# Kernel tuning notes

Hardware: AMD Instinct MI355X
Metric: run time of the kernel (lower is better)

Reference implementation:

```python
import jax, jax.numpy as jnp
import numpy as np

C = 256
NUM_HEADS = 8
FFN_HIDDEN = C * 2  # ffn_expand=2
EPS = 1e-5


def setup_inputs() -> dict:
    key = jax.random.key(0)
    ks = jax.random.split(key, 12)
    B, H, W = 16, 64, 64
    s = 0.02
    return {
        "optical": jax.random.normal(ks[0], (B, C, H, W), jnp.float32),
        "sar": jax.random.normal(ks[1], (B, C, H, W), jnp.float32),
        "g_opt": jnp.ones((C,), jnp.float32),
        "b_opt": jnp.zeros((C,), jnp.float32),
        "g_sar": jnp.ones((C,), jnp.float32),
        "b_sar": jnp.zeros((C,), jnp.float32),
        "Wq": jax.random.normal(ks[2], (C, C), jnp.float32) * s,
        "Wk": jax.random.normal(ks[3], (C, C), jnp.float32) * s,
        "Wv": jax.random.normal(ks[4], (C, C), jnp.float32) * s,
        "Wo": jax.random.normal(ks[5], (C, C), jnp.float32) * s,
        "g_ffn": jnp.ones((C,), jnp.float32),
        "b_ffn": jnp.zeros((C,), jnp.float32),
        "W1": jax.random.normal(ks[6], (2 * FFN_HIDDEN, C), jnp.float32) * s,
        "b1": jnp.zeros((2 * FFN_HIDDEN,), jnp.float32),
        "W2": jax.random.normal(ks[7], (C, FFN_HIDDEN), jnp.float32) * s,
        "b2": jnp.zeros((C,), jnp.float32),
    }


def _ln(x, g, b):
    # LayerNorm over channel axis of (B, C, H, W), biased variance, eps=1e-5
    mu = jnp.mean(x, axis=1, keepdims=True)
    var = jnp.mean(jnp.square(x - mu), axis=1, keepdims=True)
    xn = (x - mu) * jax.lax.rsqrt(var + EPS)
    return xn * g[None, :, None, None] + b[None, :, None, None]


def _proj(x, Wmat):
    # 1x1 conv == channel matmul
    return jnp.einsum('oc,bchw->bohw', Wmat, x)


def reference(optical, sar, g_opt, b_opt, g_sar, b_sar, Wq, Wk, Wv, Wo,
              g_ffn, b_ffn, W1, b1, W2, b2):
    B, Cc, H, W = optical.shape
    hc = Cc // NUM_HEADS
    L = H * W
    scale = hc ** -0.5

    opt_n = _ln(optical, g_opt, b_opt)
    sar_n = _ln(sar, g_sar, b_sar)

    # channel (transposed) attention: contraction over spatial L
    q = _proj(opt_n, Wq).reshape(B, NUM_HEADS, hc, L)
    k = _proj(sar_n, Wk).reshape(B, NUM_HEADS, hc, L)
    v = _proj(sar_n, Wv).reshape(B, NUM_HEADS, hc, L)
    A = jax.nn.softmax(jnp.einsum('bhcl,bhdl->bhcd', q, k) * scale, axis=-1)
    attn = jnp.einsum('bhcd,bhdl->bhcl', A, v).reshape(B, Cc, H, W)
    x = optical + _proj(attn, Wo)

    # SimpleGate FFN
    h = _ln(x, g_ffn, b_ffn)
    h = _proj(h, W1) + b1[None, :, None, None]
    h1, h2 = jnp.split(h, 2, axis=1)
    h = _proj(h1 * h2, W2) + b2[None, :, None, None]
    return x + h
```

## Files before the change

kernel.cpp:

```cpp
#include <hip/hip_runtime.h>
#include <hip/hip_bf16.h>

typedef __bf16 bf16;
typedef __attribute__((ext_vector_type(8))) __bf16 bf16x8;
typedef __attribute__((ext_vector_type(4))) __bf16 bf16x4;
typedef __attribute__((ext_vector_type(4))) float f32x4;
typedef __attribute__((ext_vector_type(16))) float f32x16;

#define LSP 4096
#define CCH 256

__device__ __forceinline__ void gl2lds16(const bf16* g, bf16* l) {
  __builtin_amdgcn_global_load_lds(
      (const __attribute__((address_space(1))) unsigned int*)g,
      (__attribute__((address_space(3))) unsigned int*)l, 16, 0, 0);
}

__device__ __forceinline__ f32x4 mfma16(bf16x8 a, bf16x8 b, f32x4 c) {
  return __builtin_amdgcn_mfma_f32_16x16x32_bf16(a, b, c, 0, 0, 0);
}
__device__ __forceinline__ f32x16 mfma32(bf16x8 a, bf16x8 b, f32x16 c) {
  return __builtin_amdgcn_mfma_f32_32x32x16_bf16(a, b, c, 0, 0, 0);
}

__global__ __launch_bounds__(256) void cvt_w_kernel(
    const float* __restrict__ wq, const float* __restrict__ wk,
    const float* __restrict__ wv, const float* __restrict__ wo,
    const float* __restrict__ w1, const float* __restrict__ w2,
    bf16* __restrict__ out) {
  int e = blockIdx.x * 256 + threadIdx.x;
  if (e < 65536)        { out[e] = (bf16)wq[e]; }
  else if (e < 131072)  { out[e] = (bf16)wk[e - 65536]; }
  else if (e < 196608)  {
    int e2 = e - 131072;
    int och = e2 >> 8, cin = e2 & 255;
    out[131072 + cin * 256 + och] = (bf16)wv[e2];
  }
  else if (e < 262144)  { out[e] = (bf16)wo[e - 196608]; }
  else if (e < 524288)  {
    int e2 = e - 262144;
    int m = e2 >> 8, k = e2 & 255;
    int mp = (m < 512) ? (2 * m) : (2 * (m - 512) + 1);
    out[262144 + mp * 256 + k] = (bf16)w1[e2];
  }
  else                  { out[e] = (bf16)w2[e - 524288]; }
}

__global__ __launch_bounds__(256) void ln_cl_kernel(
    const float* __restrict__ x, const float* __restrict__ gam,
    const float* __restrict__ bet, bf16* __restrict__ out_cl) {
  int p = blockIdx.x * 256 + threadIdx.x;
  int b = p >> 12, l = p & 4095;
  const float* px = x + (size_t)b * CCH * LSP + l;
  float s = 0.f, s2 = 0.f;
  #pragma unroll 16
  for (int c = 0; c < CCH; ++c) {
    float v = px[(size_t)c * LSP];
    s += v; s2 += v * v;
  }
  float mean = s * (1.f / 256.f);
  float var  = s2 * (1.f / 256.f) - mean * mean;
  float rs   = rsqrtf(var + 1e-5f);
  bf16* po = out_cl + (size_t)b * CCH * LSP + l;
  #pragma unroll 16
  for (int c = 0; c < CCH; ++c) {
    float v = px[(size_t)c * LSP];
    po[(size_t)c * LSP] = (bf16)((v - mean) * rs * gam[c] + bet[c]);
  }
}

__global__ __launch_bounds__(256) void ln_dual_kernel(
    const float* __restrict__ x, const float* __restrict__ gam,
    const float* __restrict__ bet, bf16* __restrict__ out_cl,
    bf16* __restrict__ out_lc) {
  int p = blockIdx.x * 256 + threadIdx.x;
  int b = p >> 12, l = p & 4095;
  const float* px = x + (size_t)b * CCH * LSP + l;
  float s = 0.f, s2 = 0.f;
  #pragma unroll 16
  for (int c = 0; c < CCH; ++c) {
    float v = px[(size_t)c * LSP];
    s += v; s2 += v * v;
  }
  float mean = s * (1.f / 256.f);
  float var  = s2 * (1.f / 256.f) - mean * mean;
  float rs   = rsqrtf(var + 1e-5f);
  bf16* pcl = out_cl + (size_t)b * CCH * LSP + l;
  bf16* plc = out_lc + (size_t)p * CCH;
  #pragma unroll 8
  for (int c0 = 0; c0 < CCH; c0 += 4) {
    bf16x4 o;
    #pragma unroll
    for (int i = 0; i < 4; ++i) {
      float v = px[(size_t)(c0 + i) * LSP];
      bf16 r = (bf16)((v - mean) * rs * gam[c0 + i] + bet[c0 + i]);
      o[i] = r;
      pcl[(size_t)(c0 + i) * LSP] = r;
    }
    *(bf16x4*)&plc[c0] = o;
  }
}

__global__ __launch_bounds__(256) void gram_kernel(
    const bf16* __restrict__ sar_cl, const bf16* __restrict__ opt_cl,
    float* __restrict__ part) {
  const int tile = blockIdx.x, chunk = blockIdx.y, b = blockIdx.z;
  const int tid = threadIdx.x, lane = tid & 63, w = tid >> 6;
  const int j0 = (tile >> 1) * 128 + (w >> 1) * 64;
  const int i0 = (tile & 1) * 128 + (w & 1) * 64;
  const int l0 = chunk * 1024;
  const bf16* sj = sar_cl + ((size_t)b * CCH + j0 + (lane & 31)) * LSP + l0;
  const bf16* oi = opt_cl + ((size_t)b * CCH + i0 + (lane & 31)) * LSP + l0;
  f32x16 acc[2][2];
  #pragma unroll
  for (int mt = 0; mt < 2; ++mt)
    #pragma unroll
    for (int nt = 0; nt < 2; ++nt)
      #pragma unroll
      for (int r = 0; r < 16; ++r) acc[mt][nt][r] = 0.f;
  #pragma unroll 4
  for (int ks = 0; ks < 64; ++ks) {
    int lofs = ks * 16 + (lane >> 5) * 8;
    bf16x8 a0 = *(const bf16x8*)&sj[lofs];
    bf16x8 a1 = *(const bf16x8*)&sj[32 * LSP + lofs];
    bf16x8 b0 = *(const bf16x8*)&oi[lofs];
    bf16x8 b1 = *(const bf16x8*)&oi[32 * LSP + lofs];
    acc[0][0] = mfma32(a0, b0, acc[0][0]);
    acc[0][1] = mfma32(a0, b1, acc[0][1]);
    acc[1][0] = mfma32(a1, b0, acc[1][0]);
    acc[1][1] = mfma32(a1, b1, acc[1][1]);
  }
  float* op = part + ((size_t)chunk * 16 + b) * 65536;
  #pragma unroll
  for (int mt = 0; mt < 2; ++mt)
    #pragma unroll
    for (int nt = 0; nt < 2; ++nt)
      #pragma unroll
      for (int r = 0; r < 16; ++r) {
        int row = j0 + mt * 32 + (r & 3) + 8 * (r >> 2) + 4 * (lane >> 5);
        int col = i0 + nt * 32 + (lane & 31);
        op[(size_t)row * 256 + col] = acc[mt][nt][r];
      }
}

__global__ __launch_bounds__(256) void greduce_kernel(
    const float* __restrict__ part, bf16* __restrict__ G2) {
  size_t e = ((size_t)blockIdx.x * 256 + threadIdx.x) * 8;
  float a[8];
  #pragma unroll
  for (int i = 0; i < 8; ++i) a[i] = 0.f;
  #pragma unroll
  for (int ch = 0; ch < 4; ++ch) {
    f32x4 p0 = *(const f32x4*)&part[ch * 1048576ull + e];
    f32x4 p1 = *(const f32x4*)&part[ch * 1048576ull + e + 4];
    #pragma unroll
    for (int i = 0; i < 4; ++i) { a[i] += p0[i]; a[4 + i] += p1[i]; }
  }
  bf16x8 o;
  #pragma unroll
  for (int i = 0; i < 8; ++i) o[i] = (bf16)a[i];
  *(bf16x8*)&G2[e] = o;
}

__global__ __launch_bounds__(256) void fold2_kernel(
    const bf16* __restrict__ G2, const bf16* __restrict__ Wq,
    const bf16* __restrict__ Wk, const bf16* __restrict__ WvT,
    bf16* __restrict__ UT) {
  const int bh = blockIdx.x;
  const int b = bh >> 3, h = bh & 7;
  const int tid = threadIdx.x, lane = tid & 63, w = tid >> 6;
  __shared__ bf16 M1[32 * 256];
  __shared__ float Sp[4][1024];
  __shared__ float S[1024];
  __shared__ bf16 P[1024];

  const bf16* gq = Wq + (size_t)(h * 32) * 256;
  const bf16* g2b = G2 + (size_t)b * 65536;
  #pragma unroll
  for (int mt = 0; mt < 2; ++mt)
    #pragma unroll
    for (int nt = 0; nt < 4; ++nt) {
      f32x4 acc = {0.f, 0.f, 0.f, 0.f};
      #pragma unroll
      for (int ks = 0; ks < 8; ++ks) {
        bf16x8 a = *(const bf16x8*)&gq[(size_t)(mt * 16 + (lane & 15)) * 256 +
                                       ks * 32 + (lane >> 4) * 8];
        bf16x8 bb = *(const bf16x8*)&g2b[
            (size_t)(w * 64 + nt * 16 + (lane & 15)) * 256 + ks * 32 +
            (lane >> 4) * 8];
        acc = mfma16(a, bb, acc);
      }
      #pragma unroll
      for (int r = 0; r < 4; ++r)
        M1[(mt * 16 + (lane >> 4) * 4 + r) * 256 + w * 64 + nt * 16 +
           (lane & 15)] = (bf16)acc[r];
    }
  __syncthreads();

  const bf16* gk = Wk + (size_t)(h * 32) * 256;
  #pragma unroll
  for (int mt = 0; mt < 2; ++mt)
    #pragma unroll
    for (int dt = 0; dt < 2; ++dt) {
      f32x4 acc = {0.f, 0.f, 0.f, 0.f};
      #pragma unroll
      for (int kk = 0; kk < 2; ++kk) {
        bf16x8 a = *(const bf16x8*)&M1[(mt * 16 + (lane & 15)) * 256 + w * 64 +
                                       kk * 32 + (lane >> 4) * 8];
        bf16x8 bb = *(const bf16x8*)&gk[(size_t)(dt * 16 + (lane & 15)) * 256 +
                                        w * 64 + kk * 32 + (lane >> 4) * 8];
        acc = mfma16(a, bb, acc);
      }
      #pragma unroll
      for (int r = 0; r < 4; ++r)
        Sp[w][(mt * 16 + (lane >> 4) * 4 + r) * 32 + dt * 16 + (lane & 15)] =
            acc[r];
    }
  __syncthreads();
  #pragma unroll
  for (int i = 0; i < 4; ++i) {
    int e = tid + 256 * i;
    S[e] = (Sp[0][e] + Sp[1][e] + Sp[2][e] + Sp[3][e]) * 0.17677669529663687f;
  }
  __syncthreads();
  if (tid < 32) {
    float m = -1e30f;
    #pragma unroll
    for (int d = 0; d < 32; ++d) m = fmaxf(m, S[tid * 32 + d]);
    float sum = 0.f;
    float ex[32];
    #pragma unroll
    for (int d = 0; d < 32; ++d) {
      ex[d] = __expf(S[tid * 32 + d] - m);
      sum += ex[d];
    }
    float inv = 1.f / sum;
    #pragma unroll
    for (int d = 0; d < 32; ++d) P[tid * 32 + d] = (bf16)(ex[d] * inv);
  }
  __syncthreads();

  bf16x8 bfrag[2];
  #pragma unroll
  for (int ct = 0; ct < 2; ++ct)
    bfrag[ct] =
        *(const bf16x8*)&P[(ct * 16 + (lane & 15)) * 32 + (lane >> 4) * 8];
  bf16* outb = UT + (size_t)b * 65536 + h * 32;
  #pragma unroll
  for (int t = 0; t < 4; ++t) {
    int cin16 = w * 64 + t * 16;
    bf16x8 afrag = *(const bf16x8*)&WvT[(size_t)(cin16 + (lane & 15)) * 256 +
                                        h * 32 + (lane >> 4) * 8];
    #pragma unroll
    for (int ct = 0; ct < 2; ++ct) {
      f32x4 acc = {0.f, 0.f, 0.f, 0.f};
      acc = mfma16(afrag, bfrag[ct], acc);
      int c = ct * 16 + (lane & 15);
      int cinr = cin16 + (lane >> 4) * 4;
      #pragma unroll
      for (int r = 0; r < 4; ++r)
        outb[(size_t)(cinr + r) * 256 + c] = (bf16)acc[r];
    }
  }
}

__global__ __launch_bounds__(256) void wfold_kernel(
    const bf16* __restrict__ Aw, const bf16* __restrict__ Bx,
    bf16* __restrict__ outp) {
  const int tid = threadIdx.x;
  const int lane = tid & 63;
  const int wave = tid >> 6;
  const int wr = wave >> 1, wc = wave & 1;
  const int l0 = blockIdx.x * 128;
  const int m0 = blockIdx.y * 128;
  const int b  = blockIdx.z;
  constexpr int NB = 4096;
  __shared__ bf16 smem[4 * NB];
  bf16* As = smem;
  bf16* Bs = smem + 2 * NB;
  const bf16* Ag = Aw + (size_t)m0 * 256;
  const bf16* Bg = Bx + ((size_t)b * 256 + l0) * 256;
  auto stage = [&](int buf, int k0) {
    #pragma unroll
    for (int i = 0; i < 2; ++i) {
      int ch = i * 256 + tid;
      int r  = ch >> 2;
      int c8 = (ch & 3) * 8;
      gl2lds16(Ag + (size_t)r * 256 + k0 + c8, As + buf * NB + ch * 8);
      gl2lds16(Bg + (size_t)r * 256 + k0 + c8, Bs + buf * NB + ch * 8);
    }
  };
  f32x4 acc[4][4];
  #pragma unroll
  for (int mi = 0; mi < 4; ++mi)
    #pragma unroll
    for (int ni = 0; ni < 4; ++ni)
      #pragma unroll
      for (int r = 0; r < 4; ++r) acc[mi][ni][r] = 0.f;
  stage(0, 0);
  for (int kt = 0; kt < 8; ++kt) {
    __syncthreads();
    if (kt + 1 < 8) stage((kt + 1) & 1, (kt + 1) * 32);
    const bf16* Ab = As + (kt & 1) * NB;
    const bf16* Bb = Bs + (kt & 1) * NB;
    bf16x8 af[4], bfr[4];
    #pragma unroll
    for (int mi = 0; mi < 4; ++mi)
      af[mi] = *(const bf16x8*)&Ab[(wr * 64 + mi * 16 + (lane & 15)) * 32 +
                                   (lane >> 4) * 8];
    #pragma unroll
    for (int ni = 0; ni < 4; ++ni)
      bfr[ni] = *(const bf16x8*)&Bb[(wc * 64 + ni * 16 + (lane & 15)) * 32 +
                                    (lane >> 4) * 8];
    #pragma unroll
    for (int mi = 0; mi < 4; ++mi)
      #pragma unroll
      for (int ni = 0; ni < 4; ++ni)
        acc[mi][ni] = mfma16(af[mi], bfr[ni], acc[mi][ni]);
  }
  const int mq = m0 + wr * 64 + (lane >> 4) * 4;
  const int lq = l0 + wc * 64 + (lane & 15);
  #pragma unroll
  for (int mi = 0; mi < 4; ++mi)
    #pragma unroll
    for (int ni = 0; ni < 4; ++ni) {
      int l = lq + ni * 16, mb = mq + mi * 16;
      #pragma unroll
      for (int r = 0; r < 4; ++r)
        outp[((size_t)b * 256 + mb + r) * 256 + l] = (bf16)acc[mi][ni][r];
    }
}

__global__ __launch_bounds__(256) void xgemm_ln_kernel(
    const bf16* __restrict__ Wfold, const bf16* __restrict__ sar_lc,
    const float* __restrict__ optical, const float* __restrict__ gff,
    const float* __restrict__ bff, float* __restrict__ xbuf,
    bf16* __restrict__ hn) {
  const int tid = threadIdx.x, lane = tid & 63, w = tid >> 6;
  const int l0 = blockIdx.x * 64;
  const int b  = blockIdx.y;
  __shared__ bf16 As[2][256 * 32];
  __shared__ bf16 Bs[2][64 * 32];
  __shared__ float red[2][4][64];

  const bf16* Ag = Wfold + (size_t)b * 65536;
  const bf16* Bg = sar_lc + ((size_t)b * LSP + l0) * CCH;

  auto stage = [&](int buf, int k0) {
    #pragma unroll
    for (int i = 0; i < 4; ++i) {
      int ch = i * 256 + tid;
      int r = ch >> 2, c8 = (ch & 3) * 8;
      gl2lds16(Ag + (size_t)r * 256 + k0 + c8, &As[buf][ch * 8]);
    }
    {
      int r = tid >> 2, c8 = (tid & 3) * 8;
      gl2lds16(Bg + (size_t)r * 256 + k0 + c8, &Bs[buf][tid * 8]);
    }
  };

  f32x4 acc[4][4];
  #pragma unroll
  for (int mi = 0; mi < 4; ++mi)
    #pragma unroll
    for (int ni = 0; ni < 4; ++ni)
      #pragma unroll
      for (int r = 0; r < 4; ++r) acc[mi][ni][r] = 0.f;

  stage(0, 0);
  for (int kt = 0; kt < 8; ++kt) {
    __syncthreads();
    if (kt < 7) stage((kt + 1) & 1, (kt + 1) * 32);
    const bf16* Ab = As[kt & 1];
    const bf16* Bb = Bs[kt & 1];
    bf16x8 af[4], bfr[4];
    #pragma unroll
    for (int mi = 0; mi < 4; ++mi)
      af[mi] = *(const bf16x8*)&Ab[(w * 64 + mi * 16 + (lane & 15)) * 32 +
                                   (lane >> 4) * 8];
    #pragma unroll
    for (int ni = 0; ni < 4; ++ni)
      bfr[ni] = *(const bf16x8*)&Bb[(ni * 16 + (lane & 15)) * 32 +
                                    (lane >> 4) * 8];
    #pragma unroll
    for (int mi = 0; mi < 4; ++mi)
      #pragma unroll
      for (int ni = 0; ni < 4; ++ni)
        acc[mi][ni] = mfma16(af[mi], bfr[ni], acc[mi][ni]);
  }

  const int cb = w * 64 + (lane >> 4) * 4;
  const int lb = l0 + (lane & 15);
  float s[4], q[4];
  #pragma unroll
  for (int ni = 0; ni < 4; ++ni) { s[ni] = 0.f; q[ni] = 0.f; }
  #pragma unroll
  for (int mi = 0; mi < 4; ++mi)
    #pragma unroll
    for (int ni = 0; ni < 4; ++ni) {
      int c = cb + mi * 16, l = lb + ni * 16;
      #pragma unroll
      for (int r = 0; r < 4; ++r) {
        float v = acc[mi][ni][r] + optical[((size_t)b * CCH + c + r) * LSP + l];
        acc[mi][ni][r] = v;
        s[ni] += v; q[ni] += v * v;
      }
    }
  #pragma unroll
  for (int ni = 0; ni < 4; ++ni) {
    s[ni] += __shfl_xor(s[ni], 16);
    s[ni] += __shfl_xor(s[ni], 32);
    q[ni] += __shfl_xor(q[ni], 16);
    q[ni] += __shfl_xor(q[ni], 32);
  }
  if ((lane >> 4) == 0) {
    #pragma unroll
    for (int ni = 0; ni < 4; ++ni) {
      red[0][w][ni * 16 + (lane & 15)] = s[ni];
      red[1][w][ni * 16 + (lane & 15)] = q[ni];
    }
  }
  __syncthreads();
  float mu[4], rsg[4];
  #pragma unroll
  for (int ni = 0; ni < 4; ++ni) {
    int ll = ni * 16 + (lane & 15);
    float S4 = red[0][0][ll] + red[0][1][ll] + red[0][2][ll] + red[0][3][ll];
    float Q4 = red[1][0][ll] + red[1][1][ll] + red[1][2][ll] + red[1][3][ll];
    float m = S4 * (1.f / 256.f);
    mu[ni] = m;
    rsg[ni] = rsqrtf(Q4 * (1.f / 256.f) - m * m + 1e-5f);
  }
  #pragma unroll
  for (int mi = 0; mi < 4; ++mi) {
    int c = cb + mi * 16;
    f32x4 g4 = *(const f32x4*)&gff[c];
    f32x4 b4 = *(const f32x4*)&bff[c];
    #pragma unroll
    for (int ni = 0; ni < 4; ++ni) {
      int l = lb + ni * 16;
      f32x4 xv = acc[mi][ni];
      *(f32x4*)&xbuf[((size_t)b * LSP + l) * CCH + c] = xv;
      bf16x4 o;
      #pragma unroll
      for (int r = 0; r < 4; ++r)
        o[r] = (bf16)((xv[r] - mu[ni]) * rsg[ni] * g4[r] + b4[r]);
      *(bf16x4*)&hn[((size_t)b * LSP + l) * CCH + c] = o;
    }
  }
}

template <int KEL, int MODE>
__global__ __launch_bounds__(512, 2) void ffn_gemm_kernel(
    const bf16* __restrict__ Aw, const bf16* __restrict__ Bx,
    void* __restrict__ outp, const float* __restrict__ res,
    const float* __restrict__ bias) {
  constexpr int LDSB = (MODE == 1) ? 135168 : 131072;
  __shared__ __align__(16) char smem_raw[LDSB];
  const int tid = threadIdx.x;
  const int lane = tid & 63;
  const int wave = tid >> 6;
  const int wr = wave >> 2;
  const int wc = wave & 3;
  const int l0 = blockIdx.x * 256;
  const int m0 = blockIdx.y * 256;
  const int b  = blockIdx.z;

  char* ldsA0 = smem_raw;
  char* ldsB0 = smem_raw + 32768;
  char* ldsA1 = smem_raw + 65536;
  char* ldsB1 = smem_raw + 98304;

  const bf16* Ag = Aw + (size_t)m0 * KEL;
  const bf16* Bg = Bx + ((size_t)b * LSP + l0) * KEL;

  auto STAGE = [&](const bf16* gsrc, char* ldst, int par, int kt) {
    #pragma unroll
    for (int i = 0; i < 2; ++i) {
      int qi = i * 512 + tid;
      int r  = ((qi >> 7) << 5) + (par << 4) + ((qi >> 3) & 15);
      int cl = (qi & 7) ^ ((qi >> 3) & 7);
      int p  = ((qi >> 7) << 8) + (par << 7) + (qi & 127);
      gl2lds16(gsrc + (size_t)r * KEL + kt * 64 + cl * 8,
               (bf16*)(ldst + p * 16));
    }
  };

  f32x4 acc[8][4];
  #pragma unroll
  for (int mi = 0; mi < 8; ++mi)
    #pragma unroll
    for (int ni = 0; ni < 4; ++ni)
      #pragma unroll
      for (int r = 0; r < 4; ++r) acc[mi][ni][r] = 0.f;

  bf16x8 af[4][2], bf[2][2];
  const int col0 = (((lane >> 4) << 4)) ^ ((lane & 7) << 4);
  const int col1 = col0 ^ 64;
  const int arow_off = (lane & 15) * 128;

#define LOAD_FRAGS(BUFA, BUFB, MP, NP)                                        \
  {                                                                           \
    const char* Ab_ = (BUFA);                                                 \
    const char* Bb_ = (BUFB);                                                 \
    _Pragma("unroll") for (int j = 0; j < 4; ++j) {                           \
      int rb = (wr * 128 + ((MP) + 2 * j) * 16) * 128 + arow_off;             \
      af[j][0] = *(const bf16x8*)(Ab_ + rb + col0);                           \
      af[j][1] = *(const bf16x8*)(Ab_ + rb + col1);                           \
    }                                                                         \
    _Pragma("unroll") for (int i = 0; i < 2; ++i) {                           \
      int rb = (wc * 64 + ((NP) + 2 * i) * 16) * 128 + arow_off;              \
      bf[i][0] = *(const bf16x8*)(Bb_ + rb + col0);                           \
      bf[i][1] = *(const bf16x8*)(Bb_ + rb + col1);                           \
    }                                                                         \
  }

#define DO_MFMA(MP, NP)                                                       \
  _Pragma("unroll") for (int j = 0; j < 4; ++j)                               \
  _Pragma("unroll") for (int i = 0; i < 2; ++i) {                             \
    acc[(MP) + 2 * j][(NP) + 2 * i] =                                         \
        mfma16(af[j][0], bf[i][0], acc[(MP) + 2 * j][(NP) + 2 * i]);          \
    acc[(MP) + 2 * j][(NP) + 2 * i] =                                         \
        mfma16(af[j][1], bf[i][1], acc[(MP) + 2 * j][(NP) + 2 * i]);          \
  }

#define PHASE(BUFA, BUFB, MP, NP, STG)                                        \
  asm volatile("s_waitcnt vmcnt(6)" ::: "memory");                            \
  __builtin_amdgcn_s_barrier();                                               \
  __builtin_amdgcn_sched_barrier(0);                                          \
  LOAD_FRAGS(BUFA, BUFB, MP, NP);                                             \
  STG;                                                                        \
  asm volatile("s_waitcnt lgkmcnt(0)" ::: "memory");                          \
  __builtin_amdgcn_sched_barrier(0);                                          \
  __builtin_amdgcn_s_setprio(1);                                              \
  DO_MFMA(MP, NP);                                                            \
  __builtin_amdgcn_s_setprio(0);

  STAGE(Ag, ldsA0, 0, 0);
  STAGE(Ag, ldsA0, 1, 0);
  STAGE(Bg, ldsB0, 0, 0);
  STAGE(Bg, ldsB0, 1, 0);
  STAGE(Ag, ldsA1, 0, 1);
  STAGE(Bg, ldsB1, 0, 1);

  constexpr int NITER = KEL / 128;
  for (int t = 0; t < NITER; ++t) {
    const int kt1 = 2 * t + 1;
    PHASE(ldsA0, ldsB0, 0, 0, STAGE(Ag, ldsA1, 1, kt1));
    PHASE(ldsA0, ldsB0, 0, 1, STAGE(Bg, ldsB1, 1, kt1));
    PHASE(ldsA0, ldsB0, 1, 0, STAGE(Ag, ldsA0, 0, kt1 + 1));
    PHASE(ldsA0, ldsB0, 1, 1, STAGE(Bg, ldsB0, 0, kt1 + 1));
    PHASE(ldsA1, ldsB1, 0, 0, STAGE(Ag, ldsA0, 1, kt1 + 1));
    PHASE(ldsA1, ldsB1, 0, 1, STAGE(Bg, ldsB0, 1, kt1 + 1));
    PHASE(ldsA1, ldsB1, 1, 0, STAGE(Ag, ldsA1, 0, kt1 + 2));
    PHASE(ldsA1, ldsB1, 1, 1, STAGE(Bg, ldsB1, 0, kt1 + 2));
  }
#undef PHASE
#undef DO_MFMA
#undef LOAD_FRAGS

  asm volatile("s_waitcnt vmcnt(0)" ::: "memory");
  __syncthreads();

  if constexpr (MODE == 0) {
    bf16* g_lds = (bf16*)smem_raw;
    const int lq = wc * 64 + (lane & 15);
    const int qq = (lane >> 4);
    #pragma unroll
    for (int mi = 0; mi < 8; ++mi) {
      int a0 = wr * 64 + mi * 8 + qq * 2;
      int ag = (m0 >> 1) + a0;
      float b10 = bias[ag], b1h0 = bias[ag + 512];
      float b11 = bias[ag + 1], b1h1 = bias[ag + 1 + 512];
      #pragma unroll
      for (int ni = 0; ni < 4; ++ni) {
        int l = lq + ni * 16;
        float g0 = (acc[mi][ni][0] + b10) * (acc[mi][ni][1] + b1h0);
        float g1 = (acc[mi][ni][2] + b11) * (acc[mi][ni][3] + b1h1);
        bf16 gv0 = (bf16)g0, gv1 = (bf16)g1;
        unsigned u = ((unsigned)*(unsigned short*)&gv1 << 16) |
                     (unsigned)*(unsigned short*)&gv0;
        *(unsigned*)&g_lds[l * 136 + a0] = u;
      }
    }
    __syncthreads();
    bf16* out = (bf16*)outp;
    const int gy = blockIdx.y * 128;
    #pragma unroll
    for (int it = 0; it < 8; ++it) {
      int cid = it * 512 + tid;
      int l = cid >> 4, ch = cid & 15;
      bf16x8 v = *(const bf16x8*)&g_lds[l * 136 + ch * 8];
      *(bf16x8*)&out[((size_t)b * LSP + l0 + l) * 512 + gy + ch * 8] = v;
    }
  } else {
    float* lds_f = (float*)smem_raw;
    float* out = (float*)outp;
    const int lq = wc * 64 + (lane & 15);
    const int qq = (lane >> 4);
    #pragma unroll
    for (int round = 0; round < 2; ++round) {
      if (wr == round) {
        #pragma unroll
        for (int mi = 0; mi < 8; ++mi) {
          int c0 = mi * 16 + qq * 4;
          f32x4 b4 = *(const f32x4*)&bias[round * 128 + c0];
          #pragma unroll
          for (int ni = 0; ni < 4; ++ni) {
            int l = lq + ni * 16;
            f32x4 xr = *(const f32x4*)&res[((size_t)b * LSP + l0 + l) * CCH +
                                           round * 128 + c0];
            #pragma unroll
            for (int r = 0; r < 4; ++r)
              lds_f[(c0 + r) * 260 + l] = acc[mi][ni][r] + b4[r] + xr[r];
          }
        }
      }
      __syncthreads();
      #pragma unroll
      for (int it = 0; it < 16; ++it) {
        int cid = it * 512 + tid;
        int c = cid >> 6, lch = cid & 63;
        f32x4 v = *(const f32x4*)&lds_f[c * 260 + lch * 4];
        *(f32x4*)&out[((size_t)b * CCH + round * 128 + c) * LSP + l0 +
                      lch * 4] = v;
      }
      __syncthreads();
    }
  }
}

extern "C" void kernel_launch(void* const* d_in, const int* in_sizes, int n_in,
                              void* d_out, int out_size, void* d_ws,
                              size_t ws_size, hipStream_t stream) {
  const float* optical = (const float*)d_in[0];
  const float* sar     = (const float*)d_in[1];
  const float* g_opt   = (const float*)d_in[2];
  const float* b_opt   = (const float*)d_in[3];
  const float* g_sar   = (const float*)d_in[4];
  const float* b_sar   = (const float*)d_in[5];
  const float* Wq      = (const float*)d_in[6];
  const float* Wk      = (const float*)d_in[7];
  const float* Wv      = (const float*)d_in[8];
  const float* Wo      = (const float*)d_in[9];
  const float* g_ffn   = (const float*)d_in[10];
  const float* b_ffn   = (const float*)d_in[11];
  const float* W1      = (const float*)d_in[12];
  const float* b1      = (const float*)d_in[13];
  const float* W2      = (const float*)d_in[14];
  const float* b2      = (const float*)d_in[15];

  char* ws = (char*)d_ws;
  bf16* wbf  = (bf16*)ws;
  bf16* Wqb  = wbf;
  bf16* Wkb  = wbf + 65536;
  bf16* WvTb = wbf + 131072;
  bf16* Wob  = wbf + 196608;
  bf16* W1b  = wbf + 262144;
  bf16* W2b  = wbf + 524288;

  size_t off = 2ull * 1024 * 1024;
  const size_t T16 = 16ull * LSP * CCH * 2;
  bf16* opt_ncl = (bf16*)(ws + off); off += T16;
  bf16* sar_ncl = (bf16*)(ws + off); off += T16;
  bf16* sar_nlc = (bf16*)(ws + off); off += T16;
  bf16* hn      = (bf16*)(ws + off); off += T16;
  float* xbuf   = (float*)(ws + off); off += 2 * T16;
  float* Gpart  = (float*)(ws + off); off += 16ull * 1024 * 1024;
  bf16* G2b     = (bf16*)(ws + off); off += 4ull * 1024 * 1024;
  bf16* UTb     = (bf16*)(ws + off); off += 2ull * 1024 * 1024;
  bf16* Wfoldb  = (bf16*)(ws + off); off += 2ull * 1024 * 1024;
  bf16* gbuf = opt_ncl;

  dim3 blk(256);
  cvt_w_kernel<<<2560, blk, 0, stream>>>(Wq, Wk, Wv, Wo, W1, W2, wbf);
  ln_cl_kernel<<<256, blk, 0, stream>>>(optical, g_opt, b_opt, opt_ncl);
  ln_dual_kernel<<<256, blk, 0, stream>>>(sar, g_sar, b_sar, sar_ncl, sar_nlc);
  gram_kernel<<<dim3(4, 4, 16), blk, 0, stream>>>(sar_ncl, opt_ncl, Gpart);
  greduce_kernel<<<512, blk, 0, stream>>>(Gpart, G2b);
  fold2_kernel<<<128, blk, 0, stream>>>(G2b, Wqb, Wkb, WvTb, UTb);
  wfold_kernel<<<dim3(2, 2, 16), blk, 0, stream>>>(Wob, UTb, Wfoldb);
  xgemm_ln_kernel<<<dim3(64, 16), blk, 0, stream>>>(Wfoldb, sar_nlc, optical,
                                                    g_ffn, b_ffn, xbuf, hn);
  ffn_gemm_kernel<256, 0><<<dim3(16, 4, 16), dim3(512), 0, stream>>>(
      W1b, hn, gbuf, nullptr, b1);
  ffn_gemm_kernel<512, 1><<<dim3(16, 1, 16), dim3(512), 0, stream>>>(
      W2b, gbuf, (float*)d_out, xbuf, b2);
}
```

Measured before the change: 310.2 us.

## Replace per-pixel LayerNorm kernels with LDS-tiled, vectorized, swizzled LN kernel

Result: faster. 281.7 us (-9.2%).

```diff
diff --git a/kernel.cpp b/kernel.cpp
--- a/kernel.cpp
+++ b/kernel.cpp
@@ -46,58 +46,91 @@
   else                  { out[e] = (bf16)w2[e - 524288]; }
 }
 
-__global__ __launch_bounds__(256) void ln_cl_kernel(
-    const float* __restrict__ x, const float* __restrict__ gam,
-    const float* __restrict__ bet, bf16* __restrict__ out_cl) {
-  int p = blockIdx.x * 256 + threadIdx.x;
-  int b = p >> 12, l = p & 4095;
-  const float* px = x + (size_t)b * CCH * LSP + l;
-  float s = 0.f, s2 = 0.f;
-  #pragma unroll 16
-  for (int c = 0; c < CCH; ++c) {
-    float v = px[(size_t)c * LSP];
-    s += v; s2 += v * v;
-  }
-  float mean = s * (1.f / 256.f);
-  float var  = s2 * (1.f / 256.f) - mean * mean;
-  float rs   = rsqrtf(var + 1e-5f);
-  bf16* po = out_cl + (size_t)b * CCH * LSP + l;
-  #pragma unroll 16
-  for (int c = 0; c < CCH; ++c) {
-    float v = px[(size_t)c * LSP];
-    po[(size_t)c * LSP] = (bf16)((v - mean) * rs * gam[c] + bet[c]);
-  }
-}
-
-__global__ __launch_bounds__(256) void ln_dual_kernel(
+template <int DUAL>
+__global__ __launch_bounds__(256) void ln_tile_kernel(
     const float* __restrict__ x, const float* __restrict__ gam,
     const float* __restrict__ bet, bf16* __restrict__ out_cl,
     bf16* __restrict__ out_lc) {
-  int p = blockIdx.x * 256 + threadIdx.x;
-  int b = p >> 12, l = p & 4095;
-  const float* px = x + (size_t)b * CCH * LSP + l;
-  float s = 0.f, s2 = 0.f;
-  #pragma unroll 16
-  for (int c = 0; c < CCH; ++c) {
-    float v = px[(size_t)c * LSP];
-    s += v; s2 += v * v;
-  }
-  float mean = s * (1.f / 256.f);
-  float var  = s2 * (1.f / 256.f) - mean * mean;
-  float rs   = rsqrtf(var + 1e-5f);
-  bf16* pcl = out_cl + (size_t)b * CCH * LSP + l;
-  bf16* plc = out_lc + (size_t)p * CCH;
-  #pragma unroll 8
-  for (int c0 = 0; c0 < CCH; c0 += 4) {
-    bf16x4 o;
-    #pragma unroll
-    for (int i = 0; i < 4; ++i) {
-      float v = px[(size_t)(c0 + i) * LSP];
-      bf16 r = (bf16)((v - mean) * rs * gam[c0 + i] + bet[c0 + i]);
-      o[i] = r;
-      pcl[(size_t)(c0 + i) * LSP] = r;
-    }
-    *(bf16x4*)&plc[c0] = o;
+  const int l0 = blockIdx.x * 64;
+  const int b  = blockIdx.y;
+  const int tid = threadIdx.x;
+  __shared__ bf16 Tt[256 * 64];
+  __shared__ float red[2][16][64];
+  __shared__ float mu_s[64], rs_s[64];
+
+  const float* px = x + (size_t)b * CCH * LSP + l0;
+  const int colq = (tid & 15) * 4;
+  f32x4 s = {0.f, 0.f, 0.f, 0.f}, q = {0.f, 0.f, 0.f, 0.f};
+  #pragma unroll
+  for (int it = 0; it < 16; ++it) {
+    int c = it * 16 + (tid >> 4);
+    f32x4 v = *(const f32x4*)&px[(size_t)c * LSP + colq];
+    s += v;
+    q += v * v;
+    bf16x4 h;
+    #pragma unroll
+    for (int j = 0; j < 4; ++j) h[j] = (bf16)v[j];
+    int colp = colq ^ (((c >> 3) & 7) << 3);
+    *(bf16x4*)&Tt[c * 64 + colp] = h;
+  }
+  #pragma unroll
+  for (int j = 0; j < 4; ++j) {
+    red[0][tid >> 4][colq + j] = s[j];
+    red[1][tid >> 4][colq + j] = q[j];
+  }
+  __syncthreads();
+  if (tid < 64) {
+    float S = 0.f, Q = 0.f;
+    #pragma unroll
+    for (int k = 0; k < 16; ++k) { S += red[0][k][tid]; Q += red[1][k][tid]; }
+    float m = S * (1.f / 256.f);
+    mu_s[tid] = m;
+    rs_s[tid] = rsqrtf(Q * (1.f / 256.f) - m * m + 1e-5f);
+  }
+  __syncthreads();
+
+  #pragma unroll
+  for (int it = 0; it < 8; ++it) {
+    int ch = it * 256 + tid;
+    int c = ch >> 3, col8 = (ch & 7) * 8;
+    int colp = col8 ^ (((c >> 3) & 7) << 3);
+    bf16x8 h = *(const bf16x8*)&Tt[c * 64 + colp];
+    f32x4 m0 = *(const f32x4*)&mu_s[col8];
+    f32x4 m1 = *(const f32x4*)&mu_s[col8 + 4];
+    f32x4 r0 = *(const f32x4*)&rs_s[col8];
+    f32x4 r1 = *(const f32x4*)&rs_s[col8 + 4];
+    float g = gam[c], be = bet[c];
+    bf16x8 o;
+    #pragma unroll
+    for (int j = 0; j < 4; ++j) {
+      o[j]     = (bf16)(((float)h[j] - m0[j]) * r0[j] * g + be);
+      o[4 + j] = (bf16)(((float)h[4 + j] - m1[j]) * r1[j] * g + be);
+    }
+    *(bf16x8*)&out_cl[((size_t)b * CCH + c) * LSP + l0 + col8] = o;
+  }
+
+  if constexpr (DUAL) {
+    #pragma unroll
+    for (int it = 0; it < 8; ++it) {
+      int ch = it * 256 + tid;
+      int l = ch >> 5, cch = ch & 31;
+      int c0 = cch * 8;
+      int lp = l ^ ((cch & 7) << 3);
+      float mu = mu_s[l], rs = rs_s[l];
+      f32x4 g0 = *(const f32x4*)&gam[c0];
+      f32x4 g1 = *(const f32x4*)&gam[c0 + 4];
+      f32x4 b0 = *(const f32x4*)&bet[c0];
+      f32x4 b1 = *(const f32x4*)&bet[c0 + 4];
+      bf16x8 o;
+      #pragma unroll
+      for (int j = 0; j < 4; ++j) {
+        float h0 = (float)Tt[(c0 + j) * 64 + lp];
+        float h1 = (float)Tt[(c0 + 4 + j) * 64 + lp];
+        o[j]     = (bf16)((h0 - mu) * rs * g0[j] + b0[j]);
+        o[4 + j] = (bf16)((h1 - mu) * rs * g1[j] + b1[j]);
+      }
+      *(bf16x8*)&out_lc[((size_t)b * LSP + l0 + l) * CCH + c0] = o;
+    }
   }
 }
 
@@ -380,13 +413,14 @@
                                    (lane >> 4) * 8];
     #pragma unroll
     for (int ni = 0; ni < 4; ++ni)
-      bfr[ni] = *(const bf16x8*)&Bb[(ni * 16 + (lane & 15)) * 32 +
-                                    (lane >> 4) * 8];
+      bfr[ni] = *(const bf16x8*)&Bs[kt & 1][(ni * 16 + (lane & 15)) * 32 +
+                                            (lane >> 4) * 8];
     #pragma unroll
     for (int mi = 0; mi < 4; ++mi)
       #pragma unroll
       for (int ni = 0; ni < 4; ++ni)
         acc[mi][ni] = mfma16(af[mi], bfr[ni], acc[mi][ni]);
+    (void)Bb;
   }
 
   const int cb = w * 64 + (lane >> 4) * 4;
@@ -674,8 +708,10 @@
 
   dim3 blk(256);
   cvt_w_kernel<<<2560, blk, 0, stream>>>(Wq, Wk, Wv, Wo, W1, W2, wbf);
-  ln_cl_kernel<<<256, blk, 0, stream>>>(optical, g_opt, b_opt, opt_ncl);
-  ln_dual_kernel<<<256, blk, 0, stream>>>(sar, g_sar, b_sar, sar_ncl, sar_nlc);
+  ln_tile_kernel<0><<<dim3(64, 16), blk, 0, stream>>>(optical, g_opt, b_opt,
+                                                      opt_ncl, nullptr);
+  ln_tile_kernel<1><<<dim3(64, 16), blk, 0, stream>>>(sar, g_sar, b_sar,
+                                                      sar_ncl, sar_nlc);
   gram_kernel<<<dim3(4, 4, 16), blk, 0, stream>>>(sar_ncl, opt_ncl, Gpart);
   greduce_kernel<<<512, blk, 0, stream>>>(Gpart, G2b);
   fold2_kernel<<<128, blk, 0, stream>>>(G2b, Wqb, Wkb, WvTb, UTb);
```
